# Optimization experiments

Measured on AMD Instinct MI355X. Metric: run time of the kernel, lower is better.

## Reference

```python
import jax, jax.numpy as jnp
import numpy as np

LAYERS = [1024, 2048, 1024]
OPTIONS = 4
BATCH = 2048


def setup_inputs() -> dict:
    key = jax.random.key(0)
    k_x, k_idx, k_w1, k_w2 = jax.random.split(key, 4)
    x = jax.random.normal(k_x, (BATCH, LAYERS[0]), dtype=jnp.float32)
    idx = jax.random.randint(k_idx, (BATCH,), 0, OPTIONS, dtype=jnp.int64)
    # xavier-normal-ish scaled weights per layer: shape [options, in, out]
    std1 = float(np.sqrt(2.0 / (LAYERS[0] * LAYERS[1] + OPTIONS * LAYERS[1])))
    std2 = float(np.sqrt(2.0 / (LAYERS[1] * LAYERS[2] + OPTIONS * LAYERS[2])))
    W1 = jax.random.normal(k_w1, (OPTIONS, LAYERS[0], LAYERS[1]), dtype=jnp.float32) * std1
    b1 = jnp.zeros((OPTIONS, LAYERS[1]), dtype=jnp.float32)
    W2 = jax.random.normal(k_w2, (OPTIONS, LAYERS[1], LAYERS[2]), dtype=jnp.float32) * std2
    b2 = jnp.zeros((OPTIONS, LAYERS[2]), dtype=jnp.float32)
    return {"x": x, "idx": idx, "W1": W1, "b1": b1, "W2": W2, "b2": b2}


def reference(x, idx, W1, b1, W2, b2):
    # Original: torch.bmm(x[:,None,:], W[idx]) + b[zeros_like(idx)]
    # Equivalent math without materializing the [B, in, out] gathered weights:
    # compute all options densely, then select per-sample option with idx.
    # NOTE: bias is ALWAYS option 0 (faithful to the original's zeros_like(idx)).
    def layer(h, W, b):
        h_all = jnp.einsum('bi,oij->boj', h, W)  # [B, O, out]
        h_sel = jnp.take_along_axis(h_all, idx[:, None, None], axis=1)[:, 0, :]  # [B, out]
        return h_sel + b[0][None, :]

    h = layer(x, W1, b1)
    out = layer(h, W2, b2)
    return out
```

## Files before the change

### kernel.cpp

```cpp
#include <hip/hip_runtime.h>
#include <stdint.h>

typedef __bf16 bf16x8 __attribute__((ext_vector_type(8)));
typedef float f32x4 __attribute__((ext_vector_type(4)));
typedef unsigned short u16;
typedef const __attribute__((address_space(1))) void* as1_cvp;
typedef __attribute__((address_space(3))) void* as3_vp;

__device__ __forceinline__ u16 f2bf(float f) {
  union { float f; unsigned u; } v; v.f = f;
  unsigned r = v.u + 0x7fffu + ((v.u >> 16) & 1u);
  return (u16)(r >> 16);
}

__device__ void hist_body(const int* __restrict__ idx, int n,
                          int* __restrict__ starts, int* __restrict__ perm,
                          int* __restrict__ tmap128, int* __restrict__ tmap64,
                          int* cnt , int* gmeta ) {
  int (*c4)[256] = (int(*)[256])cnt;
  int* gtot = gmeta;
  int* gstart = gmeta + 4;
  const int t = threadIdx.x;
  const int rpt = (n + 255) >> 8;
  const int base = t * rpt;
  int c[4] = {0, 0, 0, 0};
  for (int j = 0; j < rpt; ++j) {
    const int i = base + j;
    if (i < n) c[idx[i] & 3]++;
  }
  #pragma unroll
  for (int g = 0; g < 4; ++g) c4[g][t] = c[g];
  __syncthreads();
  const int w = t >> 6, l = t & 63;
  {
    const int s0 = c4[w][l * 4 + 0], s1 = c4[w][l * 4 + 1];
    const int s2 = c4[w][l * 4 + 2], s3 = c4[w][l * 4 + 3];
    const int sum = s0 + s1 + s2 + s3;
    int sc = sum;
    #pragma unroll
    for (int d = 1; d < 64; d <<= 1) {
      const int o = __shfl_up(sc, d, 64);
      if (l >= d) sc += o;
    }
    const int ex = sc - sum;
    c4[w][l * 4 + 0] = ex;
    c4[w][l * 4 + 1] = ex + s0;
    c4[w][l * 4 + 2] = ex + s0 + s1;
    c4[w][l * 4 + 3] = ex + s0 + s1 + s2;
    if (l == 63) gtot[w] = sc;
  }
  __syncthreads();
  if (t == 0) {
    int s = 0, nt128 = 0, nt64 = 0;
    for (int g = 0; g < 4; ++g) {
      gstart[g] = s;
      starts[g] = s;
      const int cg = gtot[g];
      for (int j = 0; j < cg; j += 128) tmap128[nt128++] = (g << 28) | (s + j);
      for (int j = 0; j < cg; j += 64)  tmap64[nt64++]  = (g << 28) | (s + j);
      s += cg;
    }
    starts[4] = s;
    while (nt128 < 20) tmap128[nt128++] = -1;
    while (nt64 < 40)  tmap64[nt64++]  = -1;
  }
  __syncthreads();
  int run[4] = {0, 0, 0, 0};
  for (int j = 0; j < rpt; ++j) {
    const int i = base + j;
    if (i < n) {
      const int g = idx[i] & 3;
      perm[gstart[g] + c4[g][t] + run[g]] = i;
      run[g]++;
    }
  }
}

__device__ __forceinline__ void wtrans_body(
    float (*tile)[65], const float* __restrict__ W, u16* __restrict__ WT,
    int K, int N, int tx, int ty, int o) {
  const float* Wo = W + (size_t)o * K * N;
  u16* WTo = WT + (size_t)o * N * K;
  const int k0 = ty * 64, n0 = tx * 64;
  const int rr = threadIdx.x >> 4, cc = threadIdx.x & 15;
  #pragma unroll
  for (int j = 0; j < 4; ++j) {
    const int r = j * 16 + rr;
    const float4 v = *(const float4*)(Wo + (size_t)(k0 + r) * N + n0 + cc * 4);
    tile[r][cc * 4 + 0] = v.x; tile[r][cc * 4 + 1] = v.y;
    tile[r][cc * 4 + 2] = v.z; tile[r][cc * 4 + 3] = v.w;
  }
  __syncthreads();
  #pragma unroll
  for (int j = 0; j < 4; ++j) {
    const int nrow = j * 16 + rr;
    ushort4 u;
    u.x = f2bf(tile[cc * 4 + 0][nrow]);
    u.y = f2bf(tile[cc * 4 + 1][nrow]);
    u.z = f2bf(tile[cc * 4 + 2][nrow]);
    u.w = f2bf(tile[cc * 4 + 3][nrow]);
    *(ushort4*)(WTo + (size_t)(n0 + nrow) * K + k0 + cc * 4) = u;
  }
}

__global__ __launch_bounds__(256) void w1t_hist_kernel(
    const float* __restrict__ W1, u16* __restrict__ W1T,
    const int* __restrict__ idx, int n, int* __restrict__ starts,
    int* __restrict__ perm, int* __restrict__ tmap128,
    int* __restrict__ tmap64) {
  __shared__ float tile[64][65];
  const int bid = blockIdx.x;
  if (bid == 2048) {
    hist_body(idx, n, starts, perm, tmap128, tmap64,
              (int*)&tile[0][0], (int*)&tile[32][0]);
    return;
  }
  const int xcd = bid & 7, i = bid >> 3;
  const int tx = (xcd << 2) | (i & 3);
  const int ty = (i >> 2) & 15;
  const int o = i >> 6;
  wtrans_body(tile, W1, W1T, 1024, 2048, tx, ty, o);
}

__global__ __launch_bounds__(256) void gather_kernel(
    const float* __restrict__ x, const int* __restrict__ perm,
    u16* __restrict__ Xs) {
  const int p = blockIdx.x;
  const int b = perm[p];
  const float4 v = ((const float4*)(x + (size_t)b * 1024))[threadIdx.x];
  ushort4 u;
  u.x = f2bf(v.x); u.y = f2bf(v.y); u.z = f2bf(v.z); u.w = f2bf(v.w);
  ((ushort4*)(Xs + (size_t)p * 1024))[threadIdx.x] = u;
}

template <int EPI, int TM, int NT_PAD, int KT, int NN, int NTN, int SPLIT>
__device__ __forceinline__ void gemm_body(
    char* smem, int bid,
    const u16* __restrict__ A, const u16* __restrict__ BT,
    const float* __restrict__ bias, const int* __restrict__ starts,
    const int* __restrict__ tmap, float* __restrict__ outP,
    u16* __restrict__ outH) {
  constexpr int MR = TM / 32;
  constexpr int ABUF = TM * 128;
  constexpr int BSTR = ABUF + 16384;

  const int nwg = NT_PAD * NTN * SPLIT;
  const int q = nwg >> 3;
  const int swz = (bid & 7) * q + (bid >> 3);
  const int tile = swz % NT_PAD;
  const int rest = swz / NT_PAD;
  const int n_t = rest % NTN;
  const int s = rest / NTN;

  const int tm = tmap[tile];
  if (tm < 0) return;
  const int o = tm >> 28;
  const int m_start = tm & 0x0FFFFFFF;
  const int g1 = starts[o + 1];
  const int n_start = n_t * 128;
  const int kb0 = s * (KT / SPLIT);
  const u16* Bo = BT + (size_t)o * NN * KT;

  const int tid = threadIdx.x;
  const int w = tid >> 6;
  const int l = tid & 63;
  const int wm = w >> 1, wn = w & 1;
  const int l8 = l & 7, ld8 = l >> 3;

  const int src_unit = l8 ^ (ld8 & 7);

  const u16* pA[MR];
  #pragma unroll
  for (int j = 0; j < MR; ++j) {
    int r = m_start + (j * 4 + w) * 8 + ld8;
    if (r >= g1) r = g1 - 1;
    pA[j] = A + (size_t)r * KT + kb0 + src_unit * 8;
  }
  const u16* pB[4];
  #pragma unroll
  for (int j = 0; j < 4; ++j) {
    const int nr = n_start + (j * 4 + w) * 8 + ld8;
    pB[j] = Bo + (size_t)nr * KT + kb0 + src_unit * 8;
  }

#define STAGE(dst_off)                                                         \
  {                                                                            \
    _Pragma("unroll")                                                          \
    for (int j = 0; j < MR; ++j)                                               \
      __builtin_amdgcn_global_load_lds((as1_cvp)pA[j],                         \
          (as3_vp)(smem + (dst_off) + (j * 4 + w) * 1024), 16, 0, 0);          \
    _Pragma("unroll")                                                          \
    for (int j = 0; j < 4; ++j)                                                \
      __builtin_amdgcn_global_load_lds((as1_cvp)pB[j],                         \
          (as3_vp)(smem + (dst_off) + ABUF + (j * 4 + w) * 1024), 16, 0, 0);   \
    _Pragma("unroll") for (int j = 0; j < MR; ++j) pA[j] += 64;                \
    _Pragma("unroll") for (int j = 0; j < 4; ++j) pB[j] += 64;                 \
  }

  const int lrow = l & 15;
  const int lx = l & 7;
  const int lu = l >> 4;
  int offA[MR][2], offB[4][2];
  #pragma unroll
  for (int a = 0; a < MR; ++a)
    #pragma unroll
    for (int kk = 0; kk < 2; ++kk)
      offA[a][kk] = (wm * (TM / 2) + a * 16 + lrow) * 128 + (((kk * 4 + lu) ^ lx) << 4);
  #pragma unroll
  for (int b = 0; b < 4; ++b)
    #pragma unroll
    for (int kk = 0; kk < 2; ++kk)
      offB[b][kk] = (wn * 64 + b * 16 + lrow) * 128 + (((kk * 4 + lu) ^ lx) << 4);

  f32x4 acc[MR][4] = {};

  const int nK = (KT / SPLIT) >> 6;
  STAGE(0);
  for (int kt = 0; kt < nK; ++kt) {
    const int cur = (kt & 1) * BSTR;
    if (kt + 1 < nK) {
      STAGE(BSTR - cur);
      if constexpr (TM == 128)
        asm volatile("s_waitcnt vmcnt(8)" ::: "memory");
      else
        asm volatile("s_waitcnt vmcnt(6)" ::: "memory");
    } else {
      asm volatile("s_waitcnt vmcnt(0)" ::: "memory");
    }
    __builtin_amdgcn_s_barrier();

    bf16x8 af[MR][2], bfr[4][2];
    #pragma unroll
    for (int a = 0; a < MR; ++a)
      #pragma unroll
      for (int kk = 0; kk < 2; ++kk)
        af[a][kk] = *(const bf16x8*)(smem + cur + offA[a][kk]);
    #pragma unroll
    for (int b = 0; b < 4; ++b)
      #pragma unroll
      for (int kk = 0; kk < 2; ++kk)
        bfr[b][kk] = *(const bf16x8*)(smem + cur + ABUF + offB[b][kk]);
    asm volatile("s_waitcnt lgkmcnt(0)" ::: "memory");
    __builtin_amdgcn_s_barrier();

    __builtin_amdgcn_s_setprio(1);
    #pragma unroll
    for (int kk = 0; kk < 2; ++kk)
      #pragma unroll
      for (int a = 0; a < MR; ++a)
        #pragma unroll
        for (int b = 0; b < 4; ++b)
          acc[a][b] = __builtin_amdgcn_mfma_f32_16x16x32_bf16(af[a][kk], bfr[b][kk], acc[a][b], 0, 0, 0);
    __builtin_amdgcn_s_setprio(0);
  }
#undef STAGE

  const int col_l = l & 15;
  const int row_l = (l >> 4) << 2;
  #pragma unroll
  for (int a = 0; a < MR; ++a) {
    #pragma unroll
    for (int b = 0; b < 4; ++b) {
      const int n = n_start + wn * 64 + b * 16 + col_l;
      float bv = 0.f;
      if (EPI == 0) bv = bias[n];
      #pragma unroll
      for (int r = 0; r < 4; ++r) {
        const int p = m_start + wm * (TM / 2) + a * 16 + row_l + r;
        if (p < g1) {
          if (EPI == 0) {
            outH[(size_t)p * NN + n] = f2bf(acc[a][b][r] + bv);
          } else {
            outP[((size_t)(s * 2048 + p)) * NN + n] = acc[a][b][r];
          }
        }
      }
    }
  }
}

__global__ __launch_bounds__(256, 2) void gemm1_w2t_kernel(
    const u16* __restrict__ Xs, const u16* __restrict__ W1T,
    const float* __restrict__ b1, const int* __restrict__ starts,
    const int* __restrict__ tmap64, u16* __restrict__ Hs,
    const float* __restrict__ W2, u16* __restrict__ W2T) {
  __shared__ char smem[49152];
  const int bid = blockIdx.x;
  if (bid < 640) {
    gemm_body<0, 64, 40, 1024, 2048, 16, 1>(
        smem, bid, Xs, W1T, b1, starts, tmap64, nullptr, Hs);
  } else {
    const int b = bid - 640;
    const int xcd = b & 7, i = b >> 3;
    const int tx = (xcd << 1) | (i & 1);
    const int ty = (i >> 1) & 31;
    const int o = i >> 6;
    wtrans_body((float(*)[65])smem, W2, W2T, 2048, 1024, tx, ty, o);
  }
}

__global__ __launch_bounds__(256, 2) void gemm2s_kernel(
    const u16* __restrict__ Hs, const u16* __restrict__ W2T,
    const int* __restrict__ starts, const int* __restrict__ tmap64,
    float* __restrict__ part) {
  __shared__ char smem[49152];
  gemm_body<1, 64, 40, 2048, 1024, 8, 2>(
      smem, blockIdx.x, Hs, W2T, nullptr, starts, tmap64, part, nullptr);
}

__global__ __launch_bounds__(256) void reduce_kernel(
    const float* __restrict__ part, const float* __restrict__ b2,
    const int* __restrict__ perm, float* __restrict__ out) {
  const int p = blockIdx.x;
  const int t = threadIdx.x;
  const float4 v0 = ((const float4*)(part + (size_t)p * 1024))[t];
  const float4 v1 = ((const float4*)(part + (size_t)(2048 + p) * 1024))[t];
  const float4 bv = ((const float4*)b2)[t];
  float4 r;
  r.x = v0.x + v1.x + bv.x;
  r.y = v0.y + v1.y + bv.y;
  r.z = v0.z + v1.z + bv.z;
  r.w = v0.w + v1.w + bv.w;
  ((float4*)(out + (size_t)perm[p] * 1024))[t] = r;
}

extern "C" void kernel_launch(void* const* d_in, const int* in_sizes, int n_in,
                              void* d_out, int out_size, void* d_ws, size_t ws_size,
                              hipStream_t stream) {
  (void)n_in; (void)out_size; (void)ws_size;
  const float* x   = (const float*)d_in[0];
  const int*   idx = (const int*)d_in[1];
  const float* W1  = (const float*)d_in[2];
  const float* b1  = (const float*)d_in[3];
  const float* W2  = (const float*)d_in[4];
  const float* b2  = (const float*)d_in[5];
  float* out = (float*)d_out;

  const int B = in_sizes[1];

  char* ws = (char*)d_ws;
  u16* W1T     = (u16*)(ws);
  float* part  = (float*)(ws);
  u16* W2T     = (u16*)(ws + 16777216);
  u16* Xs      = (u16*)(ws + 33554432);
  u16* Hs      = (u16*)(ws + 37748736);
  int* perm    = (int*)(ws + 46137344);
  int* starts  = (int*)(ws + 46137344 + 8192);
  int* tmap128 = starts + 64;
  int* tmap64  = starts + 128;

  w1t_hist_kernel<<<2049, 256, 0, stream>>>(W1, W1T, idx, B, starts, perm,
                                            tmap128, tmap64);
  gather_kernel<<<B, 256, 0, stream>>>(x, perm, Xs);
  gemm1_w2t_kernel<<<640 + 2048, 256, 0, stream>>>(
      Xs, W1T, b1, starts, tmap64, Hs, W2, W2T);
  gemm2s_kernel<<<640, 256, 0, stream>>>(Hs, W2T, starts, tmap64, part);
  reduce_kernel<<<B, 256, 0, stream>>>(part, b2, perm, out);
}
```

Measured before the change: 66.80 us.

## Replace split-K partial buffer and reduce kernel with atomic adds into bias-initialized output

```diff
diff --git a/kernel.cpp b/kernel.cpp
--- a/kernel.cpp
+++ b/kernel.cpp
@@ -15,7 +15,7 @@
 
 __device__ void hist_body(const int* __restrict__ idx, int n,
                           int* __restrict__ starts, int* __restrict__ perm,
-                          int* __restrict__ tmap128, int* __restrict__ tmap64,
+                          int* __restrict__ tmap64,
                           int* cnt , int* gmeta ) {
   int (*c4)[256] = (int(*)[256])cnt;
   int* gtot = gmeta;
@@ -51,18 +51,16 @@
   }
   __syncthreads();
   if (t == 0) {
-    int s = 0, nt128 = 0, nt64 = 0;
+    int s = 0, nt64 = 0;
     for (int g = 0; g < 4; ++g) {
       gstart[g] = s;
       starts[g] = s;
       const int cg = gtot[g];
-      for (int j = 0; j < cg; j += 128) tmap128[nt128++] = (g << 28) | (s + j);
-      for (int j = 0; j < cg; j += 64)  tmap64[nt64++]  = (g << 28) | (s + j);
+      for (int j = 0; j < cg; j += 64) tmap64[nt64++] = (g << 28) | (s + j);
       s += cg;
     }
     starts[4] = s;
-    while (nt128 < 20) tmap128[nt128++] = -1;
-    while (nt64 < 40)  tmap64[nt64++]  = -1;
+    while (nt64 < 40) tmap64[nt64++] = -1;
   }
   __syncthreads();
   int run[4] = {0, 0, 0, 0};
@@ -76,6 +74,20 @@
   }
 }
 
+__global__ __launch_bounds__(256) void init_hist_kernel(
+    const float* __restrict__ b2, float* __restrict__ out,
+    const int* __restrict__ idx, int n, int* __restrict__ starts,
+    int* __restrict__ perm, int* __restrict__ tmap64) {
+  __shared__ int scratch[1032];
+  const int bid = blockIdx.x;
+  if (bid == 2048) {
+    hist_body(idx, n, starts, perm, tmap64, scratch, scratch + 1024);
+    return;
+  }
+  const float4 bv = ((const float4*)b2)[threadIdx.x];
+  ((float4*)(out + (size_t)bid * 1024))[threadIdx.x] = bv;
+}
+
 __device__ __forceinline__ void wtrans_body(
     float (*tile)[65], const float* __restrict__ W, u16* __restrict__ WT,
     int K, int N, int tx, int ty, int o) {
@@ -103,16 +115,19 @@
   }
 }
 
-__global__ __launch_bounds__(256) void w1t_hist_kernel(
+__global__ __launch_bounds__(256) void w1t_gather_kernel(
     const float* __restrict__ W1, u16* __restrict__ W1T,
-    const int* __restrict__ idx, int n, int* __restrict__ starts,
-    int* __restrict__ perm, int* __restrict__ tmap128,
-    int* __restrict__ tmap64) {
+    const float* __restrict__ x, const int* __restrict__ perm,
+    u16* __restrict__ Xs) {
   __shared__ float tile[64][65];
   const int bid = blockIdx.x;
-  if (bid == 2048) {
-    hist_body(idx, n, starts, perm, tmap128, tmap64,
-              (int*)&tile[0][0], (int*)&tile[32][0]);
+  if (bid >= 2048) {
+    const int p = bid - 2048;
+    const int b = perm[p];
+    const float4 v = ((const float4*)(x + (size_t)b * 1024))[threadIdx.x];
+    ushort4 u;
+    u.x = f2bf(v.x); u.y = f2bf(v.y); u.z = f2bf(v.z); u.w = f2bf(v.w);
+    ((ushort4*)(Xs + (size_t)p * 1024))[threadIdx.x] = u;
     return;
   }
   const int xcd = bid & 7, i = bid >> 3;
@@ -122,24 +137,13 @@
   wtrans_body(tile, W1, W1T, 1024, 2048, tx, ty, o);
 }
 
-__global__ __launch_bounds__(256) void gather_kernel(
-    const float* __restrict__ x, const int* __restrict__ perm,
-    u16* __restrict__ Xs) {
-  const int p = blockIdx.x;
-  const int b = perm[p];
-  const float4 v = ((const float4*)(x + (size_t)b * 1024))[threadIdx.x];
-  ushort4 u;
-  u.x = f2bf(v.x); u.y = f2bf(v.y); u.z = f2bf(v.z); u.w = f2bf(v.w);
-  ((ushort4*)(Xs + (size_t)p * 1024))[threadIdx.x] = u;
-}
-
 template <int EPI, int TM, int NT_PAD, int KT, int NN, int NTN, int SPLIT>
 __device__ __forceinline__ void gemm_body(
     char* smem, int bid,
     const u16* __restrict__ A, const u16* __restrict__ BT,
     const float* __restrict__ bias, const int* __restrict__ starts,
-    const int* __restrict__ tmap, float* __restrict__ outP,
-    u16* __restrict__ outH) {
+    const int* __restrict__ tmap, const int* __restrict__ perm,
+    u16* __restrict__ outH, float* __restrict__ outF) {
   constexpr int MR = TM / 32;
   constexpr int ABUF = TM * 128;
   constexpr int BSTR = ABUF + 16384;
@@ -271,7 +275,7 @@
           if (EPI == 0) {
             outH[(size_t)p * NN + n] = f2bf(acc[a][b][r] + bv);
           } else {
-            outP[((size_t)(s * 2048 + p)) * NN + n] = acc[a][b][r];
+            unsafeAtomicAdd(&outF[(size_t)perm[p] * NN + n], acc[a][b][r]);
           }
         }
       }
@@ -288,7 +292,7 @@
   const int bid = blockIdx.x;
   if (bid < 640) {
     gemm_body<0, 64, 40, 1024, 2048, 16, 1>(
-        smem, bid, Xs, W1T, b1, starts, tmap64, nullptr, Hs);
+        smem, bid, Xs, W1T, b1, starts, tmap64, nullptr, Hs, nullptr);
   } else {
     const int b = bid - 640;
     const int xcd = b & 7, i = b >> 3;
@@ -302,26 +306,10 @@
 __global__ __launch_bounds__(256, 2) void gemm2s_kernel(
     const u16* __restrict__ Hs, const u16* __restrict__ W2T,
     const int* __restrict__ starts, const int* __restrict__ tmap64,
-    float* __restrict__ part) {
+    const int* __restrict__ perm, float* __restrict__ out) {
   __shared__ char smem[49152];
   gemm_body<1, 64, 40, 2048, 1024, 8, 2>(
-      smem, blockIdx.x, Hs, W2T, nullptr, starts, tmap64, part, nullptr);
-}
-
-__global__ __launch_bounds__(256) void reduce_kernel(
-    const float* __restrict__ part, const float* __restrict__ b2,
-    const int* __restrict__ perm, float* __restrict__ out) {
-  const int p = blockIdx.x;
-  const int t = threadIdx.x;
-  const float4 v0 = ((const float4*)(part + (size_t)p * 1024))[t];
-  const float4 v1 = ((const float4*)(part + (size_t)(2048 + p) * 1024))[t];
-  const float4 bv = ((const float4*)b2)[t];
-  float4 r;
-  r.x = v0.x + v1.x + bv.x;
-  r.y = v0.y + v1.y + bv.y;
-  r.z = v0.z + v1.z + bv.z;
-  r.w = v0.w + v1.w + bv.w;
-  ((float4*)(out + (size_t)perm[p] * 1024))[t] = r;
+      smem, blockIdx.x, Hs, W2T, nullptr, starts, tmap64, perm, nullptr, out);
 }
 
 extern "C" void kernel_launch(void* const* d_in, const int* in_sizes, int n_in,
@@ -340,20 +328,17 @@
 
   char* ws = (char*)d_ws;
   u16* W1T     = (u16*)(ws);
-  float* part  = (float*)(ws);
   u16* W2T     = (u16*)(ws + 16777216);
   u16* Xs      = (u16*)(ws + 33554432);
   u16* Hs      = (u16*)(ws + 37748736);
   int* perm    = (int*)(ws + 46137344);
   int* starts  = (int*)(ws + 46137344 + 8192);
-  int* tmap128 = starts + 64;
   int* tmap64  = starts + 128;
 
-  w1t_hist_kernel<<<2049, 256, 0, stream>>>(W1, W1T, idx, B, starts, perm,
-                                            tmap128, tmap64);
-  gather_kernel<<<B, 256, 0, stream>>>(x, perm, Xs);
+  init_hist_kernel<<<2049, 256, 0, stream>>>(b2, out, idx, B, starts, perm,
+                                             tmap64);
+  w1t_gather_kernel<<<4096, 256, 0, stream>>>(W1, W1T, x, perm, Xs);
   gemm1_w2t_kernel<<<640 + 2048, 256, 0, stream>>>(
       Xs, W1T, b1, starts, tmap64, Hs, W2, W2T);
-  gemm2s_kernel<<<640, 256, 0, stream>>>(Hs, W2T, starts, tmap64, part);
-  reduce_kernel<<<B, 256, 0, stream>>>(part, b2, perm, out);
-}
+  gemm2s_kernel<<<640, 256, 0, stream>>>(Hs, W2T, starts, tmap64, perm, out);
+}
```

Result: slower. 74.95 us (+12.2%).

## Fuse gather into prep kernel with per-row redundant rank computation

Applied to the files above, without the earlier changes.

```diff
diff --git a/kernel.cpp b/kernel.cpp
--- a/kernel.cpp
+++ b/kernel.cpp
@@ -15,7 +15,7 @@
 
 __device__ void hist_body(const int* __restrict__ idx, int n,
                           int* __restrict__ starts, int* __restrict__ perm,
-                          int* __restrict__ tmap128, int* __restrict__ tmap64,
+                          int* __restrict__ tmap64,
                           int* cnt , int* gmeta ) {
   int (*c4)[256] = (int(*)[256])cnt;
   int* gtot = gmeta;
@@ -51,18 +51,16 @@
   }
   __syncthreads();
   if (t == 0) {
-    int s = 0, nt128 = 0, nt64 = 0;
+    int s = 0, nt64 = 0;
     for (int g = 0; g < 4; ++g) {
       gstart[g] = s;
       starts[g] = s;
       const int cg = gtot[g];
-      for (int j = 0; j < cg; j += 128) tmap128[nt128++] = (g << 28) | (s + j);
-      for (int j = 0; j < cg; j += 64)  tmap64[nt64++]  = (g << 28) | (s + j);
+      for (int j = 0; j < cg; j += 64) tmap64[nt64++] = (g << 28) | (s + j);
       s += cg;
     }
     starts[4] = s;
-    while (nt128 < 20) tmap128[nt128++] = -1;
-    while (nt64 < 40)  tmap64[nt64++]  = -1;
+    while (nt64 < 40) tmap64[nt64++] = -1;
   }
   __syncthreads();
   int run[4] = {0, 0, 0, 0};
@@ -103,16 +101,62 @@
   }
 }
 
-__global__ __launch_bounds__(256) void w1t_hist_kernel(
+__global__ __launch_bounds__(256) void prep_kernel(
     const float* __restrict__ W1, u16* __restrict__ W1T,
-    const int* __restrict__ idx, int n, int* __restrict__ starts,
-    int* __restrict__ perm, int* __restrict__ tmap128,
-    int* __restrict__ tmap64) {
+    const float* __restrict__ x, const int* __restrict__ idx, int n,
+    int* __restrict__ starts, int* __restrict__ perm,
+    int* __restrict__ tmap64, u16* __restrict__ Xs) {
   __shared__ float tile[64][65];
+  __shared__ int s_p;
   const int bid = blockIdx.x;
-  if (bid == 2048) {
-    hist_body(idx, n, starts, perm, tmap128, tmap64,
+  const int t = threadIdx.x;
+
+  if (bid == 4096) {
+    hist_body(idx, n, starts, perm, tmap64,
               (int*)&tile[0][0], (int*)&tile[32][0]);
+    return;
+  }
+  if (bid >= 2048) {
+    const int b = bid - 2048;
+    const int gb = idx[b] & 3;
+    int* sa = (int*)&tile[0][0];
+    int* sl = sa + 1024;
+    const int rpt = (n + 255) >> 8;
+    const int base = t * rpt;
+    int ca[4] = {0, 0, 0, 0};
+    int cl = 0;
+    for (int j = 0; j < rpt; ++j) {
+      const int i = base + j;
+      if (i < n) {
+        const int g = idx[i] & 3;
+        ca[g]++;
+        cl += (i < b && g == gb);
+      }
+    }
+    #pragma unroll
+    for (int g = 0; g < 4; ++g) sa[g * 256 + t] = ca[g];
+    sl[t] = cl;
+    __syncthreads();
+    #pragma unroll
+    for (int s = 128; s > 0; s >>= 1) {
+      if (t < s) {
+        #pragma unroll
+        for (int g = 0; g < 4; ++g) sa[g * 256 + t] += sa[g * 256 + t + s];
+        sl[t] += sl[t + s];
+      }
+      __syncthreads();
+    }
+    if (t == 0) {
+      int st = 0;
+      for (int g = 0; g < gb; ++g) st += sa[g * 256];
+      s_p = st + sl[0];
+    }
+    __syncthreads();
+    const int p = s_p;
+    const float4 v = ((const float4*)(x + (size_t)b * 1024))[t];
+    ushort4 u;
+    u.x = f2bf(v.x); u.y = f2bf(v.y); u.z = f2bf(v.z); u.w = f2bf(v.w);
+    ((ushort4*)(Xs + (size_t)p * 1024))[t] = u;
     return;
   }
   const int xcd = bid & 7, i = bid >> 3;
@@ -120,17 +164,6 @@
   const int ty = (i >> 2) & 15;
   const int o = i >> 6;
   wtrans_body(tile, W1, W1T, 1024, 2048, tx, ty, o);
-}
-
-__global__ __launch_bounds__(256) void gather_kernel(
-    const float* __restrict__ x, const int* __restrict__ perm,
-    u16* __restrict__ Xs) {
-  const int p = blockIdx.x;
-  const int b = perm[p];
-  const float4 v = ((const float4*)(x + (size_t)b * 1024))[threadIdx.x];
-  ushort4 u;
-  u.x = f2bf(v.x); u.y = f2bf(v.y); u.z = f2bf(v.z); u.w = f2bf(v.w);
-  ((ushort4*)(Xs + (size_t)p * 1024))[threadIdx.x] = u;
 }
 
 template <int EPI, int TM, int NT_PAD, int KT, int NN, int NTN, int SPLIT>
@@ -346,12 +379,10 @@
   u16* Hs      = (u16*)(ws + 37748736);
   int* perm    = (int*)(ws + 46137344);
   int* starts  = (int*)(ws + 46137344 + 8192);
-  int* tmap128 = starts + 64;
   int* tmap64  = starts + 128;
 
-  w1t_hist_kernel<<<2049, 256, 0, stream>>>(W1, W1T, idx, B, starts, perm,
-                                            tmap128, tmap64);
-  gather_kernel<<<B, 256, 0, stream>>>(x, perm, Xs);
+  prep_kernel<<<4097, 256, 0, stream>>>(W1, W1T, x, idx, B, starts, perm,
+                                        tmap64, Xs);
   gemm1_w2t_kernel<<<640 + 2048, 256, 0, stream>>>(
       Xs, W1T, b1, starts, tmap64, Hs, W2, W2T);
   gemm2s_kernel<<<640, 256, 0, stream>>>(Hs, W2T, starts, tmap64, part);
```

Result: slower. 70.81 us (+6.0%).
